# Performance work log

Measured on AMD Instinct MI355X. Metric: run time of the kernel, lower is better.

## Reference

```python
import jax, jax.numpy as jnp
import numpy as np
import math

B, T = 8, 16
CODE_NUM = 1024
CODE_SIZE = 48
GRAPH_SIZE = 32
HIDDEN = 150      # hidden_size == t_output_size
T_ATTN = 32       # t_attention_size
DP_ATTN = 32      # DotProductAttention size
OUT = 1024


def _lin(k, fan_in, fan_out):
    s = 1.0 / math.sqrt(fan_in)
    kw, kb = jax.random.split(k)
    W = jax.random.uniform(kw, (fan_in, fan_out), minval=-s, maxval=s, dtype=jnp.float32)
    b = jax.random.uniform(kb, (fan_out,), minval=-s, maxval=s, dtype=jnp.float32)
    return W, b


def setup_inputs():
    key = jax.random.key(0)
    ks = jax.random.split(key, 16)
    u = jax.random.uniform(ks[0], (B, T, CODE_NUM))
    m1 = (u < 0.03).astype(jnp.float32)                   # persistent codes
    m2 = ((u >= 0.03) & (u < 0.05)).astype(jnp.float32)   # emerging neighbor codes
    m3 = ((u >= 0.05) & (u < 0.06)).astype(jnp.float32)   # emerging unrelated codes
    divided = jnp.stack([m1, m2, m3], axis=-1)            # [B,T,N,3], disjoint
    code_x = jnp.clip(m1 + m2 + m3, 0.0, 1.0)             # current-visit codes
    neighbors = ((u >= 0.06) & (u < 0.12)).astype(jnp.float32)
    lens = jax.random.randint(ks[1], (B,), T // 2, T + 1)
    a = (jax.random.uniform(ks[2], (CODE_NUM, CODE_NUM)) < 0.01).astype(jnp.float32)
    adj = a / (a.sum(axis=1, keepdims=True) + 1e-6)
    c_emb = jax.random.normal(ks[3], (CODE_NUM, CODE_SIZE)) * 0.05
    n_emb = jax.random.normal(ks[4], (CODE_NUM, CODE_SIZE)) * 0.05
    u_emb = jax.random.normal(ks[5], (CODE_NUM, GRAPH_SIZE)) * 0.05
    Wg, bg = _lin(ks[6], CODE_SIZE, GRAPH_SIZE)           # GraphLayer dense
    Wi, bi = _lin(ks[7], GRAPH_SIZE, 3 * HIDDEN)          # GRUCell input (r|z|n)
    Wh, bh = _lin(ks[8], HIDDEN, 3 * HIDDEN)              # GRUCell hidden (r|z|n)
    Wq, bq = _lin(ks[9], GRAPH_SIZE, T_ATTN)
    Wk, bk = _lin(ks[10], GRAPH_SIZE, T_ATTN)
    Wv, bv = _lin(ks[11], GRAPH_SIZE, HIDDEN)
    Wd, bd = _lin(ks[12], HIDDEN, DP_ATTN)                # DotProductAttention dense
    context = jax.random.normal(ks[13], (DP_ATTN,)) * 0.1
    Wc, bc = _lin(ks[14], HIDDEN, OUT)                    # Classifier
    return dict(code_x=code_x, divided=divided, neighbors=neighbors, lens=lens,
                adj=adj, c_emb=c_emb, n_emb=n_emb, u_emb=u_emb, Wg=Wg, bg=bg,
                Wi=Wi, bi=bi, Wh=Wh, bh=bh, Wq=Wq, bq=bq, Wk=Wk, bk=bk,
                Wv=Wv, bv=bv, Wd=Wd, bd=bd, context=context, Wc=Wc, bc=bc)


def _forward(code_x, divided, neighbors, lens, adj, c_emb, n_emb, u_emb,
             Wg, bg, Wi, bi, Wh, bh, Wq, bq, Wk, bk, Wv, bv, Wd, bd, context, Wc, bc):
    Bb, Tt, N = code_x.shape
    H = Wh.shape[0]
    NEG = -1e30
    scale = 1.0 / math.sqrt(Wq.shape[1])

    def step(carry, xs):
        h_prev, no_prev = carry                 # [B,N,H], [B,N,G]
        c_t, d_t, n_t, t_idx = xs               # [B,N], [B,N,3], [B,N], scalar
        c = c_t[..., None]
        nb = n_t[..., None]
        # GraphLayer: masked embeddings + one-hop adjacency aggregation
        ce = c * c_emb                           # [B,N,C]
        ne = nb * n_emb
        adj_ce = jnp.einsum('mn,bnc->bmc', adj, ce)
        adj_ne = jnp.einsum('mn,bnc->bmc', adj, ne)
        co = jax.nn.leaky_relu((ce + c * adj_ce + c * adj_ne) @ Wg + bg)      # [B,N,G]
        no = jax.nn.leaky_relu((ne + nb * adj_ne + nb * adj_ce) @ Wg + bg)

        m1 = d_t[..., 0]; m2 = d_t[..., 1]; m3 = d_t[..., 2]
        # TransitionLayer part 1: GRUCell on persistent (m1) codes; h_new starts at 0
        gi = co @ Wi + bi
        gh = h_prev @ Wh + bh
        i_r, i_z, i_n = jnp.split(gi, 3, axis=-1)
        h_r, h_z, h_n = jnp.split(gh, 3, axis=-1)
        r = jax.nn.sigmoid(i_r + h_r)
        z = jax.nn.sigmoid(i_z + h_z)
        n_g = jnp.tanh(i_n + r * h_n)
        h_m1 = (1.0 - z) * n_g + z * h_prev
        h_new = jnp.where(m1[..., None] > 0, h_m1, 0.0)

        # TransitionLayer part 2: single-head attention over emerging (m2|m3) codes, t>0
        m23 = (m2 + m3) > 0
        qrows = jnp.where(m2[..., None] > 0, no_prev,
                          jnp.where(m3[..., None] > 0, u_emb, 0.0))           # [B,N,G]
        q = qrows @ Wq + bq
        k = co @ Wk + bk
        v = qrows @ Wv + bv
        s = jnp.einsum('bia,bja->bij', q, k) * scale
        s = jnp.where(m23[:, None, :], s, NEG)   # keys restricted to m2|m3 set
        h_m23 = jnp.tanh(jnp.einsum('bij,bjh->bih', jax.nn.softmax(s, axis=-1), v))
        use23 = t_idx > 0
        h_new = jnp.where(jnp.logical_and(use23, m23)[..., None], h_m23, h_new)

        # per-step output: max-pool over each active subset (0 if subset empty)
        om1 = jnp.max(jnp.where(m1[..., None] > 0, h_m1, NEG), axis=1)
        om1 = jnp.where(jnp.any(m1 > 0, axis=1)[:, None], om1, 0.0)
        om23 = jnp.max(jnp.where(m23[..., None], h_m23, NEG), axis=1)
        om23 = jnp.where(jnp.logical_and(use23, jnp.any(m23, axis=1))[:, None], om23, 0.0)
        return (h_new, no), om1 + om23

    h0 = jnp.zeros((Bb, N, H), code_x.dtype)
    no0 = jnp.zeros((Bb, N, Wg.shape[1]), code_x.dtype)
    xs = (jnp.moveaxis(code_x, 1, 0), jnp.moveaxis(divided, 1, 0),
          jnp.moveaxis(neighbors, 1, 0), jnp.arange(Tt))
    _, outs = jax.lax.scan(step, (h0, no0), xs)
    outs = jnp.moveaxis(outs, 0, 1)              # [B,T,H]

    # DotProductAttention over (ragged) visit axis
    vu = (outs @ Wd + bd) @ context              # [B,T]
    tmask = jnp.arange(Tt)[None, :] < lens[:, None]
    score = jax.nn.softmax(jnp.where(tmask, vu, NEG), axis=-1)
    pooled = jnp.einsum('bth,bt->bh', outs, score)
    # Classifier (dropout_rate=0 -> identity) with sigmoid activation
    return jax.nn.sigmoid(pooled @ Wc + bc)


def reference(code_x, divided, neighbors, lens, adj, c_emb, n_emb, u_emb,
              Wg, bg, Wi, bi, Wh, bh, Wq, bq, Wk, bk, Wv, bv, Wd, bd, context, Wc, bc):
    return _forward(code_x, divided, neighbors, lens, adj, c_emb, n_emb, u_emb,
                    Wg, bg, Wi, bi, Wh, bh, Wq, bq, Wk, bk, Wv, bv, Wd, bd,
                    context, Wc, bc)
```

## Files before the change

### kernel.cpp

```cpp
#include <hip/hip_runtime.h>
#include <hip/hip_bf16.h>

#define Bq   8
#define Tq   16
#define Nq   1024
#define Cq   48
#define Gq   32
#define Hq   150
#define H3q  450
#define TAq  32
#define OUTq 1024
#define BTq  128

#define NC_CAP 128
#define NM_CAP 64
#define NACT   (2 * NC_CAP)
#define MTILE  16

__device__ __forceinline__ float lrelu(float x){ return x > 0.f ? x : 0.01f * x; }
__device__ __forceinline__ float sigm(float x){ return 1.f / (1.f + expf(-x)); }

__device__ int   g_n1[BTq], g_n23[BTq], g_nchain[BTq], g_nchain2[BTq];
__device__ short g_list1[BTq][NM_CAP];
__device__ short g_list23[BTq][NM_CAP];
__device__ short g_mapc[BTq][Nq];
__device__ short g_mapn[BTq][Nq];
__device__ int   g_chain[BTq][NM_CAP];
__device__ int   g_chain2[BTq][NM_CAP];
__device__ unsigned char g_cls[BTq][NM_CAP];
__device__ float g_Pc[Nq][Gq];
__device__ float g_Pn[Nq][Gq];
__device__ float g_co[BTq][NC_CAP][Gq];
__device__ float g_no[BTq][NC_CAP][Gq];
__device__ float g_vv[BTq][NM_CAP][Hq];
__device__ float g_hm23[BTq][NM_CAP][Hq];
__device__ float g_om23[BTq][Hq];
__device__ float g_hm1[BTq][NM_CAP][Hq];
__device__ float g_om1p[BTq][Hq];
__device__ float g_om1c[BTq][Hq];

__device__ __forceinline__ void gi3(const float* co_row, const float* Wi, const float* bi, int h,
                                    float& gr, float& gz, float& gn){
    gr = bi[h]; gz = bi[Hq + h]; gn = bi[2 * Hq + h];
    #pragma unroll
    for (int g = 0; g < Gq; ++g){
        float c = co_row[g];
        const float* w = Wi + g * H3q + h;
        gr += c * w[0];
        gz += c * w[Hq];
        gn += c * w[2 * Hq];
    }
}

__global__ __launch_bounds__(256) void k_pre(const float* c_emb, const float* n_emb, const float* Wg){
    int idx   = blockIdx.x * 256 + threadIdx.x;
    int which = idx >> 15;
    int r     = (idx >> 5) & 1023;
    int g     = idx & 31;
    const float* emb = which ? n_emb : c_emb;
    float acc = 0.f;
    for (int c = 0; c < Cq; ++c)
        acc += emb[r * Cq + c] * Wg[c * Gq + g];
    if (which) g_Pn[r][g] = acc; else g_Pc[r][g] = acc;
}

__global__ __launch_bounds__(512) void k_co(const float* code_x, const float* neighbors,
                                            const float* adj, const float* bg){
    int bt = blockIdx.x >> 1, half = blockIdx.x & 1, tid = threadIdx.x;
    __shared__ short lc_s[NC_CAP], ln_s[NC_CAP];
    __shared__ short act_s[NACT];
    __shared__ int nc_s, nn_s;
    __shared__ float Pact_s[NACT][Gq];
    __shared__ float A_s[MTILE][NACT];
    __shared__ short mrow_s[MTILE];
    int wave = tid >> 6, lane = tid & 63;

    if (wave == 0){
        int base = 0;
        for (int start = 0; start < Nq; start += 64){
            int n = start + lane;
            int pred = code_x[bt * Nq + n] > 0.f;
            unsigned long long mm = __ballot(pred);
            int pos = base + (int)__popcll(mm & ((1ull << lane) - 1ull));
            if (pred && pos < NC_CAP) lc_s[pos] = (short)n;
            base += (int)__popcll(mm);
        }
        if (lane == 0) nc_s = min(base, NC_CAP);
    } else if (wave == 1){
        int base = 0;
        for (int start = 0; start < Nq; start += 64){
            int n = start + lane;
            int pred = neighbors[bt * Nq + n] > 0.f;
            unsigned long long mm = __ballot(pred);
            int pos = base + (int)__popcll(mm & ((1ull << lane) - 1ull));
            if (pred && pos < NC_CAP) ln_s[pos] = (short)n;
            base += (int)__popcll(mm);
        }
        if (lane == 0) nn_s = min(base, NC_CAP);
    } else {
        if (half == 0) for (int n = tid - 128; n < Nq; n += 384) g_mapc[bt][n] = -1;
        else           for (int n = tid - 128; n < Nq; n += 384) g_mapn[bt][n] = -1;
    }
    __syncthreads();
    int nc = nc_s, nn = nn_s, total = nc + nn;

    for (int i = tid; i < total; i += 512) act_s[i] = (i < nc) ? lc_s[i] : ln_s[i - nc];
    if (half == 0) for (int i = tid; i < nc; i += 512) g_mapc[bt][lc_s[i]] = (short)i;
    else           for (int i = tid; i < nn; i += 512) g_mapn[bt][ln_s[i]] = (short)i;
    __syncthreads();

    for (int idx = tid; idx < total * Gq; idx += 512){
        int i = idx >> 5, g = idx & 31;
        Pact_s[i][g] = (i < nc) ? g_Pc[act_s[i]][g] : g_Pn[act_s[i]][g];
    }
    __syncthreads();

    int g = tid & 31, grp = tid >> 5;
    float bgv = bg[g];
    for (int rbase = half; rbase < total; rbase += 2 * MTILE){
        if (tid < MTILE){
            int r = rbase + 2 * tid;
            mrow_s[tid] = (r < total) ? act_s[r] : 0;
        }
        __syncthreads();
        int ntile = min(MTILE, (total - rbase + 1) / 2);
        for (int idx = tid; idx < ntile * total; idx += 512){
            int ti = idx / total, j = idx % total;
            A_s[ti][j] = adj[(size_t)mrow_s[ti] * Nq + act_s[j]];
        }
        __syncthreads();
        if (grp < ntile){
            int r = rbase + 2 * grp;
            float agg = 0.f;
            #pragma unroll 4
            for (int j = 0; j < total; ++j) agg += A_s[grp][j] * Pact_s[j][g];
            float v = lrelu(Pact_s[r][g] + agg + bgv);
            if (r < nc) g_co[bt][r][g]      = v;
            else        g_no[bt][r - nc][g] = v;
        }
        __syncthreads();
    }
}

__global__ __launch_bounds__(512) void k_mid(const float* divided, const float* u_emb,
                                             const float* Wk, const float* bk,
                                             const float* Wq_, const float* bq_,
                                             const float* Wv_, const float* bv_,
                                             const float* bg){
    int bt = blockIdx.x, tid = threadIdx.x;
    int t = bt % Tq, btp = bt - 1;
    __shared__ short l1_s[NM_CAP], l23_s[NM_CAP];
    __shared__ int n1_s, n23_s;
    __shared__ float co23_s[NM_CAP][Gq];
    __shared__ float qr_s[NM_CAP][Gq];
    __shared__ float q_s[NM_CAP][TAq + 1];
    __shared__ float k_s[NM_CAP][TAq + 1];
    __shared__ float s_s[NM_CAP][NM_CAP + 1];
    int wave = tid >> 6, lane = tid & 63;

    if (wave == 0){
        int base = 0;
        for (int start = 0; start < Nq; start += 64){
            int n = start + lane;
            int pred = divided[((size_t)bt * Nq + n) * 3 + 0] > 0.f;
            unsigned long long mm = __ballot(pred);
            int pos = base + (int)__popcll(mm & ((1ull << lane) - 1ull));
            if (pred && pos < NM_CAP) l1_s[pos] = (short)n;
            base += (int)__popcll(mm);
        }
        if (lane == 0) n1_s = min(base, NM_CAP);
    } else if (wave == 1){
        int base = 0;
        for (int start = 0; start < Nq; start += 64){
            int n = start + lane;
            float m2 = divided[((size_t)bt * Nq + n) * 3 + 1];
            float m3 = divided[((size_t)bt * Nq + n) * 3 + 2];
            int pred = (m2 > 0.f) || (m3 > 0.f);
            unsigned long long mm = __ballot(pred);
            int pos = base + (int)__popcll(mm & ((1ull << lane) - 1ull));
            if (pred && pos < NM_CAP) l23_s[pos] = (short)(n | (m2 > 0.f ? 0x400 : 0));
            base += (int)__popcll(mm);
        }
        if (lane == 0) n23_s = min(base, NM_CAP);
    }
    __syncthreads();
    int n1 = n1_s, n23 = n23_s;
    for (int i = tid; i < n1;  i += 512) g_list1[bt][i]  = l1_s[i];
    for (int i = tid; i < n23; i += 512) g_list23[bt][i] = l23_s[i];
    if (tid == 0){ g_n1[bt] = n1; g_n23[bt] = n23; }
    if (t == 0 || n23 == 0) return;

    for (int idx = tid; idx < n23 * Gq; idx += 512){
        int i = idx >> 5, g = idx & 31;
        co23_s[i][g] = g_co[bt][g_mapc[bt][l23_s[i] & 1023]][g];
    }
    for (int idx = tid; idx < n23 * Gq; idx += 512){
        int i = idx >> 5, g = idx & 31;
        int e = l23_s[i], row = e & 1023;
        float qv;
        if (e & 0x400){
            int slot = g_mapn[btp][row];
            qv = (slot >= 0) ? g_no[btp][slot][g] : lrelu(bg[g]);
        } else {
            qv = u_emb[row * Gq + g];
        }
        qr_s[i][g] = qv;
    }
    __syncthreads();
    for (int idx = tid; idx < n23 * TAq; idx += 512){
        int i = idx >> 5, a = idx & 31;
        float acck = bk[a], accq = bq_[a];
        #pragma unroll
        for (int g = 0; g < Gq; ++g){
            acck += co23_s[i][g] * Wk[g * TAq + a];
            accq += qr_s[i][g] * Wq_[g * TAq + a];
        }
        k_s[i][a] = acck; q_s[i][a] = accq;
    }
    for (int idx = tid; idx < n23 * Hq; idx += 512){
        int i = idx / Hq, h = idx % Hq;
        float acc = bv_[h];
        #pragma unroll
        for (int g = 0; g < Gq; ++g) acc += qr_s[i][g] * Wv_[g * Hq + h];
        g_vv[bt][i][h] = acc;
    }
    __syncthreads();

    const float scale = 0.17677669529663687f;
    for (int idx = tid; idx < n23 * n23; idx += 512){
        int i = idx / n23, j = idx % n23;
        float acc = 0.f;
        #pragma unroll
        for (int a = 0; a < TAq; ++a) acc += q_s[i][a] * k_s[j][a];
        s_s[i][j] = acc * scale;
    }
    __syncthreads();
    for (int i = tid; i < n23; i += 512){
        float mx = -1e30f;
        for (int j = 0; j < n23; ++j) mx = fmaxf(mx, s_s[i][j]);
        float sum = 0.f;
        for (int j = 0; j < n23; ++j){ float e = expf(s_s[i][j] - mx); s_s[i][j] = e; sum += e; }
        float inv = 1.f / sum;
        for (int j = 0; j < n23; ++j) s_s[i][j] *= inv;
    }
    __syncthreads();
    for (int idx = tid; idx < n23 * Hq; idx += 512){
        int i = idx / Hq, h = idx % Hq;
        float acc = 0.f;
        for (int j = 0; j < n23; ++j) acc += s_s[i][j] * g_vv[bt][j][h];
        g_hm23[bt][i][h] = tanhf(acc);
    }
    __syncthreads();
    for (int h = tid; h < Hq; h += 512){
        float mx = -1e30f;
        for (int i = 0; i < n23; ++i) mx = fmaxf(mx, g_hm23[bt][i][h]);
        g_om23[bt][h] = mx;
    }
}

__global__ __launch_bounds__(512) void k_gru1(const float* Wi, const float* bi,
                                              const float* Wh, const float* bh){
    int bt = blockIdx.x, tid = threadIdx.x;
    int t = bt % Tq, btp = bt - 1;
    __shared__ short map1p[Nq], map23p[Nq];
    __shared__ short l1_s[NM_CAP];
    __shared__ unsigned char cls_s[NM_CAP];
    __shared__ int m23l_s[NM_CAP];
    __shared__ int nf23_s;
    __shared__ float co1_s[NM_CAP][Gq];
    __shared__ float hb_s[Hq];
    __shared__ float ghf_s[H3q];
    __shared__ float gi_s[NM_CAP][H3q];
    int n1 = g_n1[bt];
    for (int n = tid; n < Nq; n += 512){ map1p[n] = -1; map23p[n] = -1; }
    for (int i = tid; i < n1; i += 512) l1_s[i] = g_list1[bt][i];
    __syncthreads();
    if (t >= 1){
        int n1p = g_n1[btp];
        for (int i = tid; i < n1p; i += 512) map1p[g_list1[btp][i]] = (short)i;
        if (t >= 2){
            int n23p = g_n23[btp];
            for (int i = tid; i < n23p; i += 512) map23p[g_list23[btp][i] & 1023] = (short)i;
        }
    }
    __syncthreads();
    if (tid < 64){
        int i = tid;
        int cls = 0, sp = -1;
        if (i < n1 && t >= 1){
            int row = l1_s[i];
            if (map1p[row] >= 0){ cls = 1; sp = map1p[row]; }
            else if (t >= 2 && map23p[row] >= 0){ cls = 2; sp = map23p[row]; }
        }
        if (i < n1){ cls_s[i] = (unsigned char)cls; g_cls[bt][i] = (unsigned char)cls; }
        unsigned long long mch = __ballot(cls == 1);
        unsigned long long m23 = __ballot(cls == 2);
        int pch = (int)__popcll(mch & ((1ull << i) - 1ull));
        int p23 = (int)__popcll(m23 & ((1ull << i) - 1ull));
        if (cls == 1) g_chain[bt][pch] = (i << 16) | sp;
        if (cls == 2) m23l_s[p23] = (i << 16) | sp;
        if (i == 0){ nf23_s = (int)__popcll(m23); g_nchain[bt] = (int)__popcll(mch); }
    }
    for (int idx = tid; idx < n1 * Gq; idx += 512){
        int i = idx >> 5, g = idx & 31;
        co1_s[i][g] = g_co[bt][g_mapc[bt][l1_s[i]]][g];
    }
    __syncthreads();

    if (tid < H3q){
        float wcol[Gq];
        #pragma unroll
        for (int g = 0; g < Gq; ++g) wcol[g] = Wi[g * H3q + tid];
        float bij = bi[tid];
        for (int i = 0; i < n1; ++i){
            float acc = bij;
            #pragma unroll
            for (int g = 0; g < Gq; ++g) acc += co1_s[i][g] * wcol[g];
            gi_s[i][tid] = acc;
        }
    }
    __syncthreads();

    for (int idx = tid; idx < n1 * Hq; idx += 512){
        int i = idx / Hq, h = idx % Hq;
        if (cls_s[i] != 0) continue;
        float gr = gi_s[i][h], gz = gi_s[i][Hq + h], gn = gi_s[i][2 * Hq + h];
        float r  = sigm(gr + bh[h]);
        float z  = sigm(gz + bh[Hq + h]);
        float ng = tanhf(gn + r * bh[2 * Hq + h]);
        gi_s[i][h] = (1.f - z) * ng;
    }
    __syncthreads();

    int nf23 = nf23_s;
    for (int f = 0; f < nf23; ++f){
        int pk = m23l_s[f]; int i = pk >> 16, sp = pk & 0xffff;
        for (int h = tid; h < Hq; h += 512) hb_s[h] = g_hm23[btp][sp][h];
        __syncthreads();
        for (int j = tid; j < H3q; j += 512){
            float acc = bh[j];
            for (int k2 = 0; k2 < Hq; ++k2) acc += hb_s[k2] * Wh[k2 * H3q + j];
            ghf_s[j] = acc;
        }
        __syncthreads();
        for (int h = tid; h < Hq; h += 512){
            float gr = gi_s[i][h], gz = gi_s[i][Hq + h], gn = gi_s[i][2 * Hq + h];
            float r  = sigm(gr + ghf_s[h]);
            float z  = sigm(gz + ghf_s[Hq + h]);
            float ng = tanhf(gn + r * ghf_s[2 * Hq + h]);
            gi_s[i][h] = (1.f - z) * ng + z * hb_s[h];
        }
        __syncthreads();
    }

    for (int idx = tid; idx < n1 * Hq; idx += 512){
        int i = idx / Hq, h = idx % Hq;
        if (cls_s[i] != 1) g_hm1[bt][i][h] = gi_s[i][h];
    }
    for (int h = tid; h < Hq; h += 512){
        float mx = -1e30f;
        for (int i = 0; i < n1; ++i) if (cls_s[i] != 1) mx = fmaxf(mx, gi_s[i][h]);
        g_om1p[bt][h] = mx;
    }
}

__global__ __launch_bounds__(512) void k_gru1b(const float* Wi, const float* bi,
                                               const float* Wh, const float* bh){
    int bt = blockIdx.x, tid = threadIdx.x;
    int t = bt % Tq, btp = bt - 1;
    __shared__ unsigned char defer_s[NM_CAP];
    __shared__ float co_s[Gq];
    __shared__ float hb_s[Hq];
    __shared__ float ghf_s[H3q];
    __shared__ float cmax_s[Hq];
    int nch = (t > 0) ? g_nchain[bt] : 0;
    for (int h = tid; h < Hq; h += 512) cmax_s[h] = -1e30f;
    if (tid < 64){
        int c = tid;
        int defer = 0;
        if (c < nch){
            int sp = g_chain[bt][c] & 0xffff;
            defer = (g_cls[btp][sp] == 1) ? 1 : 0;
            defer_s[c] = (unsigned char)defer;
        }
        unsigned long long md = __ballot((c < nch) && defer);
        int pos = (int)__popcll(md & ((1ull << c) - 1ull));
        if ((c < nch) && defer) g_chain2[bt][pos] = g_chain[bt][c];
        if (c == 0) g_nchain2[bt] = (int)__popcll(md);
    }
    __syncthreads();
    for (int c = 0; c < nch; ++c){
        if (defer_s[c]) continue;
        int pk = g_chain[bt][c]; int i = pk >> 16, sp = pk & 0xffff;
        if (tid < Gq) co_s[tid] = g_co[bt][g_mapc[bt][g_list1[bt][i]]][tid];
        for (int h = tid; h < Hq; h += 512) hb_s[h] = g_hm1[btp][sp][h];
        __syncthreads();
        for (int j = tid; j < H3q; j += 512){
            float acc = bh[j];
            for (int k2 = 0; k2 < Hq; ++k2) acc += hb_s[k2] * Wh[k2 * H3q + j];
            ghf_s[j] = acc;
        }
        __syncthreads();
        for (int h = tid; h < Hq; h += 512){
            float gr, gz, gn;
            gi3(co_s, Wi, bi, h, gr, gz, gn);
            float r  = sigm(gr + ghf_s[h]);
            float z  = sigm(gz + ghf_s[Hq + h]);
            float ng = tanhf(gn + r * ghf_s[2 * Hq + h]);
            float v  = (1.f - z) * ng + z * hb_s[h];
            g_hm1[bt][i][h] = v;
            cmax_s[h] = fmaxf(cmax_s[h], v);
        }
        __syncthreads();
    }
    for (int h = tid; h < Hq; h += 512) g_om1c[bt][h] = cmax_s[h];
}

__global__ __launch_bounds__(512) void k_gru2f(const float* Wi, const float* bi,
                                               const float* Wh, const float* bh,
                                               const int* lens, const float* Wd, const float* bd,
                                               const float* ctx, const float* Wc, const float* bc,
                                               float* out){
    int b = blockIdx.x, tid = threadIdx.x;
    __shared__ float co_s[Gq];
    __shared__ float hb_s[Hq];
    __shared__ float ghf_s[H3q];
    __shared__ float outs_s[Tq][Hq];
    __shared__ float wdc_s[Hq];
    __shared__ float score_s[Tq];
    __shared__ float pooled_s[Hq];
    for (int t = 1; t < Tq; ++t){
        int bt = b * Tq + t, btp = bt - 1;
        int nch2 = g_nchain2[bt];
        for (int c = 0; c < nch2; ++c){
            int pk = g_chain2[bt][c]; int i = pk >> 16, sp = pk & 0xffff;
            if (tid < Gq) co_s[tid] = g_co[bt][g_mapc[bt][g_list1[bt][i]]][tid];
            for (int h = tid; h < Hq; h += 512) hb_s[h] = g_hm1[btp][sp][h];
            __syncthreads();
            for (int j = tid; j < H3q; j += 512){
                float acc = bh[j];
                for (int k2 = 0; k2 < Hq; ++k2) acc += hb_s[k2] * Wh[k2 * H3q + j];
                ghf_s[j] = acc;
            }
            __syncthreads();
            for (int h = tid; h < Hq; h += 512){
                float gr, gz, gn;
                gi3(co_s, Wi, bi, h, gr, gz, gn);
                float r  = sigm(gr + ghf_s[h]);
                float z  = sigm(gz + ghf_s[Hq + h]);
                float ng = tanhf(gn + r * ghf_s[2 * Hq + h]);
                g_hm1[bt][i][h] = (1.f - z) * ng + z * hb_s[h];
            }
            __syncthreads();
        }
    }
    for (int idx = tid; idx < Tq * Hq; idx += 512){
        int t = idx / Hq, h = idx % Hq;
        int bt = b * Tq + t;
        int n1 = g_n1[bt], n23 = (t > 0) ? g_n23[bt] : 0;
        float o = 0.f;
        if (n1 > 0){
            float mx = fmaxf(g_om1p[bt][h], g_om1c[bt][h]);
            int nd = (t > 0) ? g_nchain2[bt] : 0;
            for (int c = 0; c < nd; ++c){
                int i = g_chain2[bt][c] >> 16;
                mx = fmaxf(mx, g_hm1[bt][i][h]);
            }
            o = mx;
        }
        if (n23 > 0) o += g_om23[bt][h];
        outs_s[t][h] = o;
    }
    for (int h = tid; h < Hq; h += 512){
        float acc = 0.f;
        for (int d = 0; d < 32; ++d) acc += Wd[h * 32 + d] * ctx[d];
        wdc_s[h] = acc;
    }
    __syncthreads();
    int len = lens[b];
    if (tid < Tq){
        int t = tid;
        float acc = 0.f;
        for (int d = 0; d < 32; ++d) acc += bd[d] * ctx[d];
        for (int h = 0; h < Hq; ++h) acc += outs_s[t][h] * wdc_s[h];
        score_s[t] = (t < len) ? acc : -1e30f;
    }
    __syncthreads();
    if (tid == 0){
        float mx = -1e30f;
        for (int t = 0; t < Tq; ++t) mx = fmaxf(mx, score_s[t]);
        float sum = 0.f;
        for (int t = 0; t < Tq; ++t){ float e = expf(score_s[t] - mx); score_s[t] = e; sum += e; }
        float inv = 1.f / sum;
        for (int t = 0; t < Tq; ++t) score_s[t] *= inv;
    }
    __syncthreads();
    for (int h = tid; h < Hq; h += 512){
        float acc = 0.f;
        for (int t = 0; t < Tq; ++t) acc += score_s[t] * outs_s[t][h];
        pooled_s[h] = acc;
    }
    __syncthreads();
    for (int o = tid; o < OUTq; o += 512){
        float acc = bc[o];
        for (int h = 0; h < Hq; ++h) acc += pooled_s[h] * Wc[h * OUTq + o];
        out[b * OUTq + o] = sigm(acc);
    }
}

extern "C" void kernel_launch(void* const* d_in, const int* in_sizes, int n_in,
                              void* d_out, int out_size, void* d_ws, size_t ws_size,
                              hipStream_t stream){
    const float* code_x    = (const float*)d_in[0];
    const float* divided   = (const float*)d_in[1];
    const float* neighbors = (const float*)d_in[2];
    const int*   lens      = (const int*)  d_in[3];
    const float* adj       = (const float*)d_in[4];
    const float* c_emb     = (const float*)d_in[5];
    const float* n_emb     = (const float*)d_in[6];
    const float* u_emb     = (const float*)d_in[7];
    const float* Wg        = (const float*)d_in[8];
    const float* bg        = (const float*)d_in[9];
    const float* Wi        = (const float*)d_in[10];
    const float* bi        = (const float*)d_in[11];
    const float* Wh        = (const float*)d_in[12];
    const float* bh        = (const float*)d_in[13];
    const float* Wq_       = (const float*)d_in[14];
    const float* bq_       = (const float*)d_in[15];
    const float* Wk_       = (const float*)d_in[16];
    const float* bk_       = (const float*)d_in[17];
    const float* Wv_       = (const float*)d_in[18];
    const float* bv_       = (const float*)d_in[19];
    const float* Wd_       = (const float*)d_in[20];
    const float* bd_       = (const float*)d_in[21];
    const float* ctx       = (const float*)d_in[22];
    const float* Wc_       = (const float*)d_in[23];
    const float* bc_       = (const float*)d_in[24];
    float* out = (float*)d_out;

    hipLaunchKernelGGL(k_pre,   dim3(256),     dim3(256), 0, stream, c_emb, n_emb, Wg);
    hipLaunchKernelGGL(k_co,    dim3(2 * BTq), dim3(512), 0, stream, code_x, neighbors, adj, bg);
    hipLaunchKernelGGL(k_mid,   dim3(BTq),     dim3(512), 0, stream, divided, u_emb,
                       Wk_, bk_, Wq_, bq_, Wv_, bv_, bg);
    hipLaunchKernelGGL(k_gru1,  dim3(BTq),     dim3(512), 0, stream, Wi, bi, Wh, bh);
    hipLaunchKernelGGL(k_gru1b, dim3(BTq),     dim3(512), 0, stream, Wi, bi, Wh, bh);
    hipLaunchKernelGGL(k_gru2f, dim3(Bq),      dim3(512), 0, stream, Wi, bi, Wh, bh,
                       lens, Wd_, bd_, ctx, Wc_, bc_, out);
}
```

Baseline: 284.1 us.

## Keep attention values in LDS, stage mask flags, write only reused hidden rows

The k_mid kernel now stages the divided mask into shared-memory byte flags with a coalesced load, so the ballot scans no longer do strided global reads. The V projection and tanh attention output stay in LDS instead of round-tripping through global g_vv and g_hm23. g_hm23 rows are written only for codes that become persistent at the next step (wm flag). This adds about 76KB of LDS per block, which may lower occupancy, and depends on downstream kernels reading only those rows.

```diff
diff --git a/kernel.cpp b/kernel.cpp
--- a/kernel.cpp
+++ b/kernel.cpp
@@ -32,7 +32,6 @@
 __device__ float g_Pn[Nq][Gq];
 __device__ float g_co[BTq][NC_CAP][Gq];
 __device__ float g_no[BTq][NC_CAP][Gq];
-__device__ float g_vv[BTq][NM_CAP][Hq];
 __device__ float g_hm23[BTq][NM_CAP][Hq];
 __device__ float g_om23[BTq][Hq];
 __device__ float g_hm1[BTq][NM_CAP][Hq];
@@ -149,21 +148,34 @@
                                              const float* bg){
     int bt = blockIdx.x, tid = threadIdx.x;
     int t = bt % Tq, btp = bt - 1;
+    __shared__ unsigned char f1_s[Nq], f2_s[Nq], f3_s[Nq];
     __shared__ short l1_s[NM_CAP], l23_s[NM_CAP];
+    __shared__ unsigned char wm_s[NM_CAP];
     __shared__ int n1_s, n23_s;
     __shared__ float co23_s[NM_CAP][Gq];
     __shared__ float qr_s[NM_CAP][Gq];
     __shared__ float q_s[NM_CAP][TAq + 1];
     __shared__ float k_s[NM_CAP][TAq + 1];
     __shared__ float s_s[NM_CAP][NM_CAP + 1];
+    __shared__ float vv_s[NM_CAP][Hq];
+    __shared__ float hm_s[NM_CAP][Hq];
     int wave = tid >> 6, lane = tid & 63;
 
+    for (int idx = tid; idx < Nq * 3; idx += 512){
+        float v = divided[(size_t)bt * Nq * 3 + idx];
+        int n = idx / 3, c = idx - n * 3;
+        unsigned char f = (v > 0.f) ? 1 : 0;
+        if (c == 0) f1_s[n] = f;
+        else if (c == 1) f2_s[n] = f;
+        else f3_s[n] = f;
+    }
+    __syncthreads();
     if (wave == 0){
         int base = 0;
         for (int start = 0; start < Nq; start += 64){
             int n = start + lane;
-            int pred = divided[((size_t)bt * Nq + n) * 3 + 0] > 0.f;
-            unsigned long long mm = __ballot(pred);
+            int pred = f1_s[n];
+            unsigned long long mm = __ballot(pred != 0);
             int pos = base + (int)__popcll(mm & ((1ull << lane) - 1ull));
             if (pred && pos < NM_CAP) l1_s[pos] = (short)n;
             base += (int)__popcll(mm);
@@ -173,12 +185,11 @@
         int base = 0;
         for (int start = 0; start < Nq; start += 64){
             int n = start + lane;
-            float m2 = divided[((size_t)bt * Nq + n) * 3 + 1];
-            float m3 = divided[((size_t)bt * Nq + n) * 3 + 2];
-            int pred = (m2 > 0.f) || (m3 > 0.f);
-            unsigned long long mm = __ballot(pred);
+            int m2 = f2_s[n], m3 = f3_s[n];
+            int pred = m2 | m3;
+            unsigned long long mm = __ballot(pred != 0);
             int pos = base + (int)__popcll(mm & ((1ull << lane) - 1ull));
-            if (pred && pos < NM_CAP) l23_s[pos] = (short)(n | (m2 > 0.f ? 0x400 : 0));
+            if (pred && pos < NM_CAP) l23_s[pos] = (short)(n | (m2 ? 0x400 : 0));
             base += (int)__popcll(mm);
         }
         if (lane == 0) n23_s = min(base, NM_CAP);
@@ -190,6 +201,12 @@
     if (tid == 0){ g_n1[bt] = n1; g_n23[bt] = n23; }
     if (t == 0 || n23 == 0) return;
 
+    for (int i = tid; i < n23; i += 512){
+        int row = l23_s[i] & 1023;
+        unsigned char wm = 0;
+        if (t < Tq - 1) wm = (divided[((size_t)(bt + 1) * Nq + row) * 3] > 0.f) ? 1 : 0;
+        wm_s[i] = wm;
+    }
     for (int idx = tid; idx < n23 * Gq; idx += 512){
         int i = idx >> 5, g = idx & 31;
         co23_s[i][g] = g_co[bt][g_mapc[bt][l23_s[i] & 1023]][g];
@@ -222,7 +239,7 @@
         float acc = bv_[h];
         #pragma unroll
         for (int g = 0; g < Gq; ++g) acc += qr_s[i][g] * Wv_[g * Hq + h];
-        g_vv[bt][i][h] = acc;
+        vv_s[i][h] = acc;
     }
     __syncthreads();
 
@@ -247,13 +264,17 @@
     for (int idx = tid; idx < n23 * Hq; idx += 512){
         int i = idx / Hq, h = idx % Hq;
         float acc = 0.f;
-        for (int j = 0; j < n23; ++j) acc += s_s[i][j] * g_vv[bt][j][h];
-        g_hm23[bt][i][h] = tanhf(acc);
-    }
-    __syncthreads();
+        for (int j = 0; j < n23; ++j) acc += s_s[i][j] * vv_s[j][h];
+        hm_s[i][h] = tanhf(acc);
+    }
+    __syncthreads();
+    for (int idx = tid; idx < n23 * Hq; idx += 512){
+        int i = idx / Hq, h = idx % Hq;
+        if (wm_s[i]) g_hm23[bt][i][h] = hm_s[i][h];
+    }
     for (int h = tid; h < Hq; h += 512){
         float mx = -1e30f;
-        for (int i = 0; i < n23; ++i) mx = fmaxf(mx, g_hm23[bt][i][h]);
+        for (int i = 0; i < n23; ++i) mx = fmaxf(mx, hm_s[i][h]);
         g_om23[bt][h] = mx;
     }
 }
```

Measured after the change: 278.7 us. About the same (-1.9%).
